# Optimization experiments

Measured on AMD Instinct MI355X. Metric: run time of the kernel, lower is better.

Reference implementation:

```python
import jax, jax.numpy as jnp
import numpy as np

VOCAB = 100000
DIM = 128
TOTAL_TOKENS = 819200
NUM_SENTENCES = 16384
STD = 0.02


def setup_inputs() -> dict:
    key = jax.random.key(0)
    k1, k2, k3, k4 = jax.random.split(key, 4)
    tokens = jax.random.randint(k1, (TOTAL_TOKENS,), 0, VOCAB, dtype=jnp.int32)
    segment_ids = jnp.sort(
        jax.random.randint(k2, (TOTAL_TOKENS,), 0, NUM_SENTENCES, dtype=jnp.int32))
    embedding_table = jax.random.normal(k3, (VOCAB, DIM), dtype=jnp.float32) * STD
    # nn.Linear default init ~ U(-1/sqrt(dim), 1/sqrt(dim)); any init is fine for a reference
    W = jax.random.normal(k4, (DIM, DIM), dtype=jnp.float32) * (1.0 / np.sqrt(DIM))
    b = jnp.zeros((DIM,), dtype=jnp.float32)
    return {"tokens": tokens, "segment_ids": segment_ids,
            "embedding_table": embedding_table, "W": W, "b": b}


def reference(tokens, segment_ids, embedding_table, W, b):
    # Per-word embedding lookup (the recurrent_group step) ...
    emb = embedding_table[tokens]                         # [T, D]
    # ... followed by ragged sum pooling over each sentence (sequence_pooling 'sum')
    bow = jax.ops.segment_sum(emb, segment_ids,
                              num_segments=NUM_SENTENCES)  # [B, D]
    # one_more_hidden: Linear(dim, dim) + ReLU
    return jax.nn.relu(bow @ W + b)                       # [B, D]
```

## Files before the change

kernel.cpp:

```cpp
#include <hip/hip_runtime.h>
#include <hip/hip_fp16.h>

#define DIM 128
#define GROWS 32

typedef _Float16 f16x8 __attribute__((ext_vector_type(8)));
typedef float f32x4 __attribute__((ext_vector_type(4)));

__global__ __launch_bounds__(256, 2) void prep_kernel(
    const int* __restrict__ segs, int* __restrict__ seg_start,
    const float* __restrict__ emb, const float* __restrict__ W,
    signed char* __restrict__ qtab, float* __restrict__ scales,
    int T, int B, int V, int mtiles, int nTrans) {
  if ((int)blockIdx.x >= nTrans) {
    const int i = (blockIdx.x - nTrans) * 256 + threadIdx.x;
    if (i > T) return;
    const int cur = (i < T) ? segs[i] : B;
    const int prev = (i > 0) ? segs[i - 1] : -1;
    for (int s = prev + 1; s <= cur; ++s) seg_start[s] = i;
    return;
  }

  const int wid = blockIdx.x * 4 + (threadIdx.x >> 6);
  const int nwaves = nTrans * 4;
  const int lane = threadIdx.x & 63;
  const int lr = lane & 15;
  const int lg = lane >> 4;

  f16x8 bfrag[8][4];
#pragma unroll
  for (int n = 0; n < 8; ++n)
#pragma unroll
    for (int s = 0; s < 4; ++s) {
      const float* wp = W + (size_t)(s * 32 + lg * 8) * DIM + n * 16 + lr;
      f16x8 f;
#pragma unroll
      for (int i = 0; i < 8; ++i) f[i] = (_Float16)wp[(size_t)i * DIM];
      bfrag[n][s] = f;
    }

  for (int mt = wid; mt < mtiles; mt += nwaves) {
    const float* arow = emb + (size_t)(mt * 16 + lr) * DIM;
    f16x8 afrag[4];
#pragma unroll
    for (int s = 0; s < 4; ++s) {
      const float4 a0 = *reinterpret_cast<const float4*>(arow + s * 32 + lg * 8);
      const float4 a1 = *reinterpret_cast<const float4*>(arow + s * 32 + lg * 8 + 4);
      f16x8 f;
      f[0] = (_Float16)a0.x; f[1] = (_Float16)a0.y;
      f[2] = (_Float16)a0.z; f[3] = (_Float16)a0.w;
      f[4] = (_Float16)a1.x; f[5] = (_Float16)a1.y;
      f[6] = (_Float16)a1.z; f[7] = (_Float16)a1.w;
      afrag[s] = f;
    }
    f32x4 accs[8];
#pragma unroll
    for (int n = 0; n < 8; ++n) {
      f32x4 a = {0.f, 0.f, 0.f, 0.f};
#pragma unroll
      for (int s = 0; s < 4; ++s)
        a = __builtin_amdgcn_mfma_f32_16x16x32_f16(afrag[s], bfrag[n][s],
                                                   a, 0, 0, 0);
      accs[n] = a;
    }
    const int r0 = mt * 16 + lg * 4;
    float inv[4];
#pragma unroll
    for (int j = 0; j < 4; ++j) {
      float mm = fabsf(accs[0][j]);
#pragma unroll
      for (int n = 1; n < 8; ++n) mm = fmaxf(mm, fabsf(accs[n][j]));
      mm = fmaxf(mm, __shfl_xor(mm, 1));
      mm = fmaxf(mm, __shfl_xor(mm, 2));
      mm = fmaxf(mm, __shfl_xor(mm, 4));
      mm = fmaxf(mm, __shfl_xor(mm, 8));
      inv[j] = (mm > 0.f) ? 127.f / mm : 0.f;
      if (lr == 0) scales[r0 + j] = mm * (1.f / 127.f);
    }
#pragma unroll
    for (int n = 0; n < 8; ++n)
#pragma unroll
      for (int j = 0; j < 4; ++j)
        qtab[(size_t)(r0 + j) * DIM + n * 16 + lr] =
            (signed char)(int)rintf(accs[n][j] * inv[j]);
  }

  const int tailStart = mtiles * 16;
  if (wid == 0 && tailStart < V) {
    const int c2 = lane * 2;
    for (int r = tailStart; r < V; ++r) {
      float s0 = 0.f, s1 = 0.f;
      for (int k = 0; k < DIM; ++k) {
        const float e = emb[(size_t)r * DIM + k];
        s0 = fmaf(e, W[(size_t)k * DIM + c2], s0);
        s1 = fmaf(e, W[(size_t)k * DIM + c2 + 1], s1);
      }
      float mm = fmaxf(fabsf(s0), fabsf(s1));
      mm = fmaxf(mm, __shfl_xor(mm, 1));
      mm = fmaxf(mm, __shfl_xor(mm, 2));
      mm = fmaxf(mm, __shfl_xor(mm, 4));
      mm = fmaxf(mm, __shfl_xor(mm, 8));
      mm = fmaxf(mm, __shfl_xor(mm, 16));
      mm = fmaxf(mm, __shfl_xor(mm, 32));
      const float iv = (mm > 0.f) ? 127.f / mm : 0.f;
      if (lane == 0) scales[r] = mm * (1.f / 127.f);
      qtab[(size_t)r * DIM + c2] = (signed char)(int)rintf(s0 * iv);
      qtab[(size_t)r * DIM + c2 + 1] = (signed char)(int)rintf(s1 * iv);
    }
  }
}


#define ACC4(w, o, SV)                                                     \
  acc[(o) + 0] = fmaf(SV, (float)((int)((w) << 24) >> 24), acc[(o) + 0]);  \
  acc[(o) + 1] = fmaf(SV, (float)((int)((w) << 16) >> 24), acc[(o) + 1]);  \
  acc[(o) + 2] = fmaf(SV, (float)((int)((w) <<  8) >> 24), acc[(o) + 2]);  \
  acc[(o) + 3] = fmaf(SV, (float)((int)(w) >> 24),         acc[(o) + 3]);

__global__ __launch_bounds__(256, 4) void segsum_q8(
    const int* __restrict__ tokens, const signed char* __restrict__ qtab,
    const float* __restrict__ scales, const int* __restrict__ seg_start,
    const float* __restrict__ bias, float* __restrict__ out, int B) {
  const int seg = blockIdx.x * 4 + (threadIdx.x >> 6);
  if (seg >= B) return;
  const int lane = threadIdx.x & 63;
  const int g = lane >> 3;
  const int c16 = (lane & 7) * 16;
  const int lo = seg_start[seg], hi = seg_start[seg + 1];
  const int cnt = hi - lo;
  const int last = hi - 1;
  float acc[16] = {0.f, 0.f, 0.f, 0.f, 0.f, 0.f, 0.f, 0.f,
                   0.f, 0.f, 0.f, 0.f, 0.f, 0.f, 0.f, 0.f};

  const int nbatch = (cnt + 63) >> 6;
  for (int b = 0; b < nbatch; ++b) {
    const int base = lo + (b << 6);
    int idx[8], tok[8];
#pragma unroll
    for (int u = 0; u < 8; ++u) {
      idx[u] = base + 8 * u + g;
      tok[u] = tokens[min(idx[u], last)];
    }
    float sv[8];
    uint4 rv[8];
#pragma unroll
    for (int u = 0; u < 8; ++u) {
      sv[u] = (idx[u] <= last) ? scales[tok[u]] : 0.f;
      rv[u] = *reinterpret_cast<const uint4*>(
          qtab + (size_t)tok[u] * DIM + c16);
    }
#pragma unroll
    for (int u = 0; u < 8; ++u) {
      ACC4(rv[u].x, 0, sv[u])
      ACC4(rv[u].y, 4, sv[u])
      ACC4(rv[u].z, 8, sv[u])
      ACC4(rv[u].w, 12, sv[u])
    }
  }
#pragma unroll
  for (int i = 0; i < 16; ++i) {
    acc[i] += __shfl_xor(acc[i], 8);
    acc[i] += __shfl_xor(acc[i], 16);
    acc[i] += __shfl_xor(acc[i], 32);
  }
  if (g == 0) {
    const int d0 = (lane & 7) * 16;
    float* op = out + (size_t)seg * DIM + d0;
    const float* bp = bias + d0;
#pragma unroll
    for (int j = 0; j < 4; ++j) {
      const float4 bv = *reinterpret_cast<const float4*>(bp + 4 * j);
      float4 o;
      o.x = fmaxf(acc[4 * j + 0] + bv.x, 0.f);
      o.y = fmaxf(acc[4 * j + 1] + bv.y, 0.f);
      o.z = fmaxf(acc[4 * j + 2] + bv.z, 0.f);
      o.w = fmaxf(acc[4 * j + 3] + bv.w, 0.f);
      *reinterpret_cast<float4*>(op + 4 * j) = o;
    }
  }
}
#undef ACC4

__global__ __launch_bounds__(256) void boundaries_kernel(
    const int* __restrict__ segs, int* __restrict__ seg_start, int T, int B) {
  const int i = blockIdx.x * 256 + threadIdx.x;
  if (i > T) return;
  const int cur = (i < T) ? segs[i] : B;
  const int prev = (i > 0) ? segs[i - 1] : -1;
  for (int s = prev + 1; s <= cur; ++s) seg_start[s] = i;
}

#define LOADF(u, TIDX)                                                     \
  const int t##u = tokens[(TIDX)];                                         \
  const float4 e##u = *reinterpret_cast<const float4*>(                    \
      emb + (size_t)t##u * DIM + c4);
#define ADDF(u) { acc.x += e##u.x; acc.y += e##u.y; acc.z += e##u.z; acc.w += e##u.w; }

__global__ __launch_bounds__(256, 4) void segsum_f32(
    const int* __restrict__ tokens, const float* __restrict__ emb,
    const int* __restrict__ seg_start, float* __restrict__ bow, int B) {
  const int seg = blockIdx.x * 4 + (threadIdx.x >> 6);
  if (seg >= B) return;
  const int lane = threadIdx.x & 63;
  const int half = lane >> 5;
  const int c4 = (lane & 31) * 4;
  const int lo = seg_start[seg], hi = seg_start[seg + 1];
  const int cnt = hi - lo;
  float4 acc = make_float4(0.f, 0.f, 0.f, 0.f);

  int base = lo;
  const int nb = cnt >> 4;
  for (int b = 0; b < nb; ++b, base += 16) {
    LOADF(0, base + 0 + half)  LOADF(1, base + 2 + half)
    LOADF(2, base + 4 + half)  LOADF(3, base + 6 + half)
    LOADF(4, base + 8 + half)  LOADF(5, base + 10 + half)
    LOADF(6, base + 12 + half) LOADF(7, base + 14 + half)
    ADDF(0) ADDF(1) ADDF(2) ADDF(3) ADDF(4) ADDF(5) ADDF(6) ADDF(7)
  }
  if (cnt & 15) {
    const int last = hi - 1;
#define LOADT(u) const int i##u = base + 2 * u + half; LOADF(u, min(i##u, last))
    LOADT(0) LOADT(1) LOADT(2) LOADT(3)
    LOADT(4) LOADT(5) LOADT(6) LOADT(7)
    if (i0 <= last) ADDF(0)
    if (i1 <= last) ADDF(1)
    if (i2 <= last) ADDF(2)
    if (i3 <= last) ADDF(3)
    if (i4 <= last) ADDF(4)
    if (i5 <= last) ADDF(5)
    if (i6 <= last) ADDF(6)
    if (i7 <= last) ADDF(7)
#undef LOADT
  }
  acc.x += __shfl_xor(acc.x, 32);
  acc.y += __shfl_xor(acc.y, 32);
  acc.z += __shfl_xor(acc.z, 32);
  acc.w += __shfl_xor(acc.w, 32);
  if (half == 0)
    *reinterpret_cast<float4*>(bow + (size_t)seg * DIM + c4) = acc;
}

__global__ __launch_bounds__(256) void gemm_bias_relu(
    const float* __restrict__ bow, const float* __restrict__ W,
    const float* __restrict__ bias, float* __restrict__ out) {
  __shared__ float bt[GROWS][DIM];
  const int tid = threadIdx.x;
  const size_t row0 = (size_t)blockIdx.x * GROWS;

  {
    const float4* src = reinterpret_cast<const float4*>(bow + row0 * DIM);
    float4* dst = reinterpret_cast<float4*>(&bt[0][0]);
#pragma unroll
    for (int i = 0; i < (GROWS * DIM / 4) / 256; ++i)
      dst[tid + 256 * i] = src[tid + 256 * i];
  }
  __syncthreads();

  const int cg = tid & 31;
  const int rg = tid >> 5;
  const int c0 = cg * 4;

  float acc[4][4] = {};
#pragma unroll 4
  for (int k = 0; k < DIM; ++k) {
    const float4 w4 = *reinterpret_cast<const float4*>(W + (size_t)k * DIM + c0);
#pragma unroll
    for (int j = 0; j < 4; ++j) {
      const float s = bt[rg * 4 + j][k];
      acc[j][0] = fmaf(s, w4.x, acc[j][0]);
      acc[j][1] = fmaf(s, w4.y, acc[j][1]);
      acc[j][2] = fmaf(s, w4.z, acc[j][2]);
      acc[j][3] = fmaf(s, w4.w, acc[j][3]);
    }
  }

  const float4 bv = *reinterpret_cast<const float4*>(bias + c0);
#pragma unroll
  for (int j = 0; j < 4; ++j) {
    float4 o;
    o.x = fmaxf(acc[j][0] + bv.x, 0.f);
    o.y = fmaxf(acc[j][1] + bv.y, 0.f);
    o.z = fmaxf(acc[j][2] + bv.z, 0.f);
    o.w = fmaxf(acc[j][3] + bv.w, 0.f);
    *reinterpret_cast<float4*>(out + (row0 + rg * 4 + j) * DIM + c0) = o;
  }
}

extern "C" void kernel_launch(void* const* d_in, const int* in_sizes, int n_in,
                              void* d_out, int out_size, void* d_ws, size_t ws_size,
                              hipStream_t stream) {
  const int* tokens = (const int*)d_in[0];
  const int* segs = (const int*)d_in[1];
  const float* emb = (const float*)d_in[2];
  const float* W = (const float*)d_in[3];
  const float* bias = (const float*)d_in[4];
  float* out = (float*)d_out;

  const int T = in_sizes[0];
  const int B = out_size / DIM;
  const int V = in_sizes[2] / DIM;

  int* seg_start = (int*)d_ws;
  const size_t ss_bytes = ((size_t)(B + 1) * 4 + 255) & ~(size_t)255;
  const size_t sc_bytes = ((size_t)V * 4 + 255) & ~(size_t)255;

  const bool qok = ws_size >= ss_bytes + sc_bytes + (size_t)V * DIM;
  if (qok) {
    float* scales = (float*)((char*)d_ws + ss_bytes);
    signed char* qtab = (signed char*)((char*)d_ws + ss_bytes + sc_bytes);
    const int nbBound = (T + 1 + 255) / 256;
    const int NTRANS = 512;
    const int mtiles = V / 16;
    prep_kernel<<<NTRANS + nbBound, 256, 0, stream>>>(
        segs, seg_start, emb, W, qtab, scales, T, B, V, mtiles, NTRANS);
    segsum_q8<<<(B + 3) / 4, 256, 0, stream>>>(
        tokens, qtab, scales, seg_start, bias, out, B);
  } else {
    float* bow = out;
    boundaries_kernel<<<(T + 1 + 255) / 256, 256, 0, stream>>>(segs, seg_start, T, B);
    segsum_f32<<<(B + 3) / 4, 256, 0, stream>>>(tokens, emb, seg_start, bow, B);
    gemm_bias_relu<<<B / GROWS, 256, 0, stream>>>(bow, W, bias, out);
  }
}
```

Before: 46.76 us.

## Split quantized table into column slices for cache-local segment gather

Stores the int8 projected table as four 32-column slices ([4][V][32]) and launches four times as many gather blocks, each covering one column slice for a group of segments. Each slice is about 3.2MB, so block-ordered slices are meant to keep their working set resident in L2/LLC and make random gathers cheaper. In exchange, token ids and scales are read four times, each lane does smaller 8-byte loads, and there is an extra shuffle stage.

```diff
diff --git a/kernel.cpp b/kernel.cpp
--- a/kernel.cpp
+++ b/kernel.cpp
@@ -81,7 +81,7 @@
     for (int n = 0; n < 8; ++n)
 #pragma unroll
       for (int j = 0; j < 4; ++j)
-        qtab[(size_t)(r0 + j) * DIM + n * 16 + lr] =
+        qtab[((size_t)(n >> 1) * V + (r0 + j)) * 32 + (n & 1) * 16 + lr] =
             (signed char)(int)rintf(accs[n][j] * inv[j]);
   }
 
@@ -104,8 +104,10 @@
       mm = fmaxf(mm, __shfl_xor(mm, 32));
       const float iv = (mm > 0.f) ? 127.f / mm : 0.f;
       if (lane == 0) scales[r] = mm * (1.f / 127.f);
-      qtab[(size_t)r * DIM + c2] = (signed char)(int)rintf(s0 * iv);
-      qtab[(size_t)r * DIM + c2 + 1] = (signed char)(int)rintf(s1 * iv);
+      qtab[((size_t)(c2 >> 5) * V + r) * 32 + (c2 & 31)] =
+          (signed char)(int)rintf(s0 * iv);
+      qtab[((size_t)((c2 + 1) >> 5) * V + r) * 32 + ((c2 + 1) & 31)] =
+          (signed char)(int)rintf(s1 * iv);
     }
   }
 }
@@ -117,58 +119,59 @@
   acc[(o) + 2] = fmaf(SV, (float)((int)((w) <<  8) >> 24), acc[(o) + 2]);  \
   acc[(o) + 3] = fmaf(SV, (float)((int)(w) >> 24),         acc[(o) + 3]);
 
-__global__ __launch_bounds__(256, 4) void segsum_q8(
+__global__ __launch_bounds__(256, 4) void segsum_q8s(
     const int* __restrict__ tokens, const signed char* __restrict__ qtab,
     const float* __restrict__ scales, const int* __restrict__ seg_start,
-    const float* __restrict__ bias, float* __restrict__ out, int B) {
-  const int seg = blockIdx.x * 4 + (threadIdx.x >> 6);
+    const float* __restrict__ bias, float* __restrict__ out,
+    int B, int V, int NBS) {
+  const int bid = blockIdx.x;
+  const int slice = bid / NBS;
+  const int seg = (bid - slice * NBS) * 4 + (threadIdx.x >> 6);
   if (seg >= B) return;
   const int lane = threadIdx.x & 63;
-  const int g = lane >> 3;
-  const int c16 = (lane & 7) * 16;
+  const int rg = lane >> 2;
+  const int c8 = (lane & 3) * 8;
+  const signed char* qs = qtab + (size_t)slice * V * 32;
   const int lo = seg_start[seg], hi = seg_start[seg + 1];
   const int cnt = hi - lo;
   const int last = hi - 1;
-  float acc[16] = {0.f, 0.f, 0.f, 0.f, 0.f, 0.f, 0.f, 0.f,
-                   0.f, 0.f, 0.f, 0.f, 0.f, 0.f, 0.f, 0.f};
+  float acc[8] = {0.f, 0.f, 0.f, 0.f, 0.f, 0.f, 0.f, 0.f};
 
   const int nbatch = (cnt + 63) >> 6;
   for (int b = 0; b < nbatch; ++b) {
     const int base = lo + (b << 6);
-    int idx[8], tok[8];
-#pragma unroll
-    for (int u = 0; u < 8; ++u) {
-      idx[u] = base + 8 * u + g;
+    int idx[4], tok[4];
+#pragma unroll
+    for (int u = 0; u < 4; ++u) {
+      idx[u] = base + 16 * u + rg;
       tok[u] = tokens[min(idx[u], last)];
     }
-    float sv[8];
-    uint4 rv[8];
-#pragma unroll
-    for (int u = 0; u < 8; ++u) {
+    float sv[4];
+    uint2 rv[4];
+#pragma unroll
+    for (int u = 0; u < 4; ++u) {
       sv[u] = (idx[u] <= last) ? scales[tok[u]] : 0.f;
-      rv[u] = *reinterpret_cast<const uint4*>(
-          qtab + (size_t)tok[u] * DIM + c16);
-    }
-#pragma unroll
-    for (int u = 0; u < 8; ++u) {
+      rv[u] = *reinterpret_cast<const uint2*>(qs + (size_t)tok[u] * 32 + c8);
+    }
+#pragma unroll
+    for (int u = 0; u < 4; ++u) {
       ACC4(rv[u].x, 0, sv[u])
       ACC4(rv[u].y, 4, sv[u])
-      ACC4(rv[u].z, 8, sv[u])
-      ACC4(rv[u].w, 12, sv[u])
-    }
-  }
-#pragma unroll
-  for (int i = 0; i < 16; ++i) {
+    }
+  }
+#pragma unroll
+  for (int i = 0; i < 8; ++i) {
+    acc[i] += __shfl_xor(acc[i], 4);
     acc[i] += __shfl_xor(acc[i], 8);
     acc[i] += __shfl_xor(acc[i], 16);
     acc[i] += __shfl_xor(acc[i], 32);
   }
-  if (g == 0) {
-    const int d0 = (lane & 7) * 16;
+  if (rg == 0) {
+    const int d0 = slice * 32 + (lane & 3) * 8;
     float* op = out + (size_t)seg * DIM + d0;
     const float* bp = bias + d0;
 #pragma unroll
-    for (int j = 0; j < 4; ++j) {
+    for (int j = 0; j < 2; ++j) {
       const float4 bv = *reinterpret_cast<const float4*>(bp + 4 * j);
       float4 o;
       o.x = fmaxf(acc[4 * j + 0] + bv.x, 0.f);
@@ -313,8 +316,9 @@
     const int mtiles = V / 16;
     prep_kernel<<<NTRANS + nbBound, 256, 0, stream>>>(
         segs, seg_start, emb, W, qtab, scales, T, B, V, mtiles, NTRANS);
-    segsum_q8<<<(B + 3) / 4, 256, 0, stream>>>(
-        tokens, qtab, scales, seg_start, bias, out, B);
+    const int NBS = (B + 3) / 4;
+    segsum_q8s<<<4 * NBS, 256, 0, stream>>>(
+        tokens, qtab, scales, seg_start, bias, out, B, V, NBS);
   } else {
     float* bow = out;
     boundaries_kernel<<<(T + 1 + 255) / 256, 256, 0, stream>>>(segs, seg_start, T, B);
```

Result: slower. 65.04 us (+39.1%).
